# Performance work log

Measured on AMD Instinct MI355X. Metric: run time of the kernel, lower is better.

The kernel has to match this reference:

```python
import jax, jax.numpy as jnp
import numpy as np

HIDDEN = 2048
NUM_HEADS = 16
NUM_KV_HEADS = 4
HEAD_DIM = HIDDEN // NUM_HEADS  # 128
ROPE_THETA = 1000000.0
B, S = 2, 2048


def setup_inputs() -> dict:
    key = jax.random.key(0)
    ks = jax.random.split(key, 10)
    sc = 0.02
    return {
        "hidden_states": jax.random.normal(ks[0], (B, S, HIDDEN), jnp.float32),
        "position_ids": jnp.broadcast_to(jnp.arange(S, dtype=jnp.int32), (B, S)),
        "Wq": jax.random.normal(ks[1], (HIDDEN, NUM_HEADS * HEAD_DIM), jnp.float32) * sc,
        "bq": jnp.zeros((NUM_HEADS * HEAD_DIM,), jnp.float32),
        "Wk": jax.random.normal(ks[2], (HIDDEN, NUM_KV_HEADS * HEAD_DIM), jnp.float32) * sc,
        "bk": jnp.zeros((NUM_KV_HEADS * HEAD_DIM,), jnp.float32),
        "Wv": jax.random.normal(ks[3], (HIDDEN, NUM_KV_HEADS * HEAD_DIM), jnp.float32) * sc,
        "bv": jnp.zeros((NUM_KV_HEADS * HEAD_DIM,), jnp.float32),
        "Wo": jax.random.normal(ks[4], (NUM_HEADS * HEAD_DIM, HIDDEN), jnp.float32) * sc,
        "bo": jnp.zeros((HIDDEN,), jnp.float32),
    }


def _rope_cos_sin(position_ids, dtype):
    # inv_freq: [head_dim/2]
    inv_freq = 1.0 / (ROPE_THETA ** (jnp.arange(0, HEAD_DIM, 2, dtype=jnp.float32) / HEAD_DIM))
    freqs = position_ids.astype(jnp.float32)[:, :, None] * inv_freq[None, None, :]  # [B,S,d/2]
    emb = jnp.concatenate([freqs, freqs], axis=-1)  # [B,S,d]
    return jnp.cos(emb).astype(dtype), jnp.sin(emb).astype(dtype)


def _rotate_half(x):
    h = x.shape[-1] // 2
    return jnp.concatenate([-x[..., h:], x[..., :h]], axis=-1)


def _attention(hidden_states, position_ids, Wq, bq, Wk, bk, Wv, bv, Wo, bo):
    bsz, q_len, _ = hidden_states.shape
    q = (hidden_states @ Wq + bq).reshape(bsz, q_len, NUM_HEADS, HEAD_DIM).transpose(0, 2, 1, 3)
    k = (hidden_states @ Wk + bk).reshape(bsz, q_len, NUM_KV_HEADS, HEAD_DIM).transpose(0, 2, 1, 3)
    v = (hidden_states @ Wv + bv).reshape(bsz, q_len, NUM_KV_HEADS, HEAD_DIM).transpose(0, 2, 1, 3)

    cos, sin = _rope_cos_sin(position_ids, hidden_states.dtype)
    cos = cos[:, None, :, :]  # [B,1,S,d]
    sin = sin[:, None, :, :]
    q = q * cos + _rotate_half(q) * sin
    k = k * cos + _rotate_half(k) * sin

    # repeat_kv (GQA): [B,kvh,S,d] -> [B,H,S,d]
    n_rep = NUM_HEADS // NUM_KV_HEADS
    k = jnp.repeat(k, n_rep, axis=1)
    v = jnp.repeat(v, n_rep, axis=1)

    scale = 1.0 / jnp.sqrt(jnp.array(HEAD_DIM, hidden_states.dtype))
    scores = jnp.einsum('bhqd,bhkd->bhqk', q, k) * scale  # [B,H,S,S]
    causal = jnp.tril(jnp.ones((q_len, q_len), bool))
    scores = jnp.where(causal[None, None], scores, jnp.finfo(scores.dtype).min)
    probs = jax.nn.softmax(scores.astype(jnp.float32), axis=-1).astype(hidden_states.dtype)
    attn = jnp.einsum('bhqk,bhkd->bhqd', probs, v)
    attn = attn.transpose(0, 2, 1, 3).reshape(bsz, q_len, HIDDEN)
    return attn @ Wo + bo


def reference(hidden_states, position_ids, Wq, bq, Wk, bk, Wv, bv, Wo, bo):
    return _attention(hidden_states, position_ids, Wq, bq, Wk, bk, Wv, bv, Wo, bo)
```

## Files before the change

### kernel.cpp

```cpp
#include <hip/hip_runtime.h>
#include <cmath>

#define HIDDEN 2048
#define NH 16
#define NKV 4
#define HD 128
#define SEQ 2048
#define BATCH 2

typedef unsigned short ushort_t;
typedef short bf16x8 __attribute__((ext_vector_type(8)));
typedef float f32x4 __attribute__((ext_vector_type(4)));
typedef ushort_t u16x4 __attribute__((ext_vector_type(4)));

__device__ __forceinline__ ushort_t f2bf(float f) {
    union { float f; unsigned int u; } v; v.f = f;
    unsigned int r = v.u + 0x7fffu + ((v.u >> 16) & 1u);
    return (ushort_t)(r >> 16);
}
__device__ __forceinline__ ushort_t f2bf_trunc(float f) {
    union { float f; unsigned int u; } v; v.f = f;
    return (ushort_t)(v.u >> 16);
}

__device__ __forceinline__ f32x4 mfma16(bf16x8 a, bf16x8 b, f32x4 c) {
    return __builtin_amdgcn_mfma_f32_16x16x32_bf16(a, b, c, 0, 0, 0);
}

__device__ __forceinline__ void load_lds16(const void* g, void* l) {
    __builtin_amdgcn_global_load_lds((const __attribute__((address_space(1))) unsigned int*)g,
                                     (__attribute__((address_space(3))) unsigned int*)l,
                                     16, 0, 0);
}


__global__ __launch_bounds__(256) void prep(const float* __restrict__ Wq,
                                            const float* __restrict__ Wk,
                                            const float* __restrict__ Wv,
                                            const float* __restrict__ Wo,
                                            ushort_t* __restrict__ WqkvT,
                                            ushort_t* __restrict__ WoT,
                                            const float* __restrict__ hs,
                                            ushort_t* __restrict__ Xb) {
    const int z = blockIdx.z;
    const int t = threadIdx.x;
    if (z >= 4) {
        int g = (((z - 4) * 32 + blockIdx.y) * 32 + blockIdx.x) * 256 + t;
        float4 v = ((const float4*)hs)[g];
        u16x4 o;
        o[0] = f2bf(v.x); o[1] = f2bf(v.y); o[2] = f2bf(v.z); o[3] = f2bf(v.w);
        ((u16x4*)Xb)[g] = o;
        return;
    }
    const float* W;
    ushort_t* WT;
    int N;
    if (z == 0)      { W = Wq; WT = WqkvT;                        N = 2048; }
    else if (z == 1) { W = Wk; WT = WqkvT + 2048ull * 2048;       N = 512;  }
    else if (z == 2) { W = Wv; WT = WqkvT + 2560ull * 2048;       N = 512;  }
    else             { W = Wo; WT = WoT;                          N = 2048; }
    const int K = 2048;
    const int n0 = blockIdx.x * 64, k0 = blockIdx.y * 64;
    if (n0 >= N) return;
    __shared__ ushort_t T[64][72];
    for (int idx = t; idx < 64 * 16; idx += 256) {
        int r = idx >> 4, c4 = (idx & 15) << 2;
        float4 v = *(const float4*)&W[(size_t)(k0 + r) * N + n0 + c4];
        T[r][c4 + 0] = f2bf(v.x); T[r][c4 + 1] = f2bf(v.y);
        T[r][c4 + 2] = f2bf(v.z); T[r][c4 + 3] = f2bf(v.w);
    }
    __syncthreads();
    for (int idx = t; idx < 64 * 16; idx += 256) {
        int n = idx >> 4, kg = (idx & 15) << 2;
        u16x4 o;
        o[0] = T[kg + 0][n]; o[1] = T[kg + 1][n];
        o[2] = T[kg + 2][n]; o[3] = T[kg + 3][n];
        *(u16x4*)&WT[(size_t)(n0 + n) * K + k0 + kg] = o;
    }
}

template <int MODE, int BMH>
__global__ __launch_bounds__(512) void gemm256(const ushort_t* __restrict__ A,
                                               const ushort_t* __restrict__ Bt,
                                               const float* __restrict__ bias,
                                               const float* __restrict__ bias2,
                                               const float* __restrict__ bias3,
                                               void* __restrict__ out,
                                               void* __restrict__ out2,
                                               void* __restrict__ out3,
                                               int M, int N, int K,
                                               const int* __restrict__ posids) {
    constexpr int IM = 4 * BMH;
    constexpr int APL = BMH * 128 * 32;
    constexpr int BPL = 256 * 32;
    __shared__ __align__(16) ushort_t Asb[2 * 2 * APL];
    __shared__ __align__(16) ushort_t Bsb[2 * 2 * BPL];
    const int tid = threadIdx.x;
    const int w = tid >> 6, lane = tid & 63, quad = lane >> 4, l16 = lane & 15;
    const int wr = w >> 2, wc = w & 3;
    const int m0 = blockIdx.y * (128 * BMH), n0 = blockIdx.x * 256;

    f32x4 acc[IM][4];
#pragma unroll
    for (int i = 0; i < IM; i++)
#pragma unroll
        for (int j = 0; j < 4; j++)
#pragma unroll
            for (int e = 0; e < 4; e++) acc[i][j][e] = 0.0f;

    const int srow = lane >> 2;
    const int gc8 = (((lane & 3) ^ ((lane >> 3) & 3)) << 3);

    auto stageA = [&](int t, int buf, int ha) {
        const ushort_t* g = A + (size_t)(m0 + ha * 128 + w * 16 + srow) * K + t * 64 + gc8;
        ushort_t* l = &Asb[buf * 2 * APL + (ha * 128 + w * 16) * 32];
        load_lds16(g, l);
        load_lds16(g + 32, l + APL);
    };
    auto stageB = [&](int t, int buf, int ha) {
        const ushort_t* g = Bt + (size_t)(n0 + ha * 128 + w * 16 + srow) * K + t * 64 + gc8;
        ushort_t* l = &Bsb[buf * 2 * BPL + (ha * 128 + w * 16) * 32];
        load_lds16(g, l);
        load_lds16(g + 32, l + BPL);
    };

    const int slot = ((quad ^ ((l16 >> 1) & 3)) << 3);
    const int arow = (wr * (64 * BMH) + l16) * 32 + slot;
    const int brow = (wc * 16 + l16) * 32 + slot;

    const int nt = K >> 6;

    stageA(0, 0, 0);
    if constexpr (BMH == 2) stageA(0, 0, 1);
    stageB(0, 0, 0);
    stageB(0, 0, 1);
    asm volatile("s_waitcnt vmcnt(2)" ::: "memory");
    __builtin_amdgcn_s_barrier();
    __builtin_amdgcn_sched_barrier(0);

    bf16x8 a[IM];
    for (int u = 0; u < nt; ++u) {
        const int bu = u & 1, bn = bu ^ 1;
        const bool pf = (u + 1 < nt);
        const ushort_t* Ap0 = &Asb[bu * 2 * APL];
        const ushort_t* Ap1 = Ap0 + APL;
        const ushort_t* Bp0 = &Bsb[bu * 2 * BPL];
        const ushort_t* Bp1 = Bp0 + BPL;

#pragma unroll
        for (int i = 0; i < IM; i++) a[i] = *(const bf16x8*)&Ap0[arow + i * 512];
        bf16x8 b0 = *(const bf16x8*)&Bp0[brow];
        bf16x8 b1 = *(const bf16x8*)&Bp0[brow + 2048];
        if (pf) { stageA(u + 1, bn, 0); asm volatile("s_waitcnt vmcnt(2)" ::: "memory"); }
        else    { asm volatile("s_waitcnt vmcnt(0)" ::: "memory"); }
        __builtin_amdgcn_s_barrier();
        __builtin_amdgcn_sched_barrier(0);
        __builtin_amdgcn_s_setprio(1);
#pragma unroll
        for (int i = 0; i < IM; i++) {
            acc[i][0] = mfma16(a[i], b0, acc[i][0]);
            acc[i][1] = mfma16(a[i], b1, acc[i][1]);
        }
        __builtin_amdgcn_s_setprio(0);
        __builtin_amdgcn_sched_barrier(0);
        __builtin_amdgcn_s_barrier();
        __builtin_amdgcn_sched_barrier(0);

        bf16x8 b2 = *(const bf16x8*)&Bp0[brow + 4096];
        bf16x8 b3 = *(const bf16x8*)&Bp0[brow + 6144];
        if (pf) {
            if constexpr (BMH == 2) stageA(u + 1, bn, 1);
            else                    stageB(u + 1, bn, 0);
        }
        __builtin_amdgcn_s_barrier();
        __builtin_amdgcn_sched_barrier(0);
        __builtin_amdgcn_s_setprio(1);
#pragma unroll
        for (int i = 0; i < IM; i++) {
            acc[i][2] = mfma16(a[i], b2, acc[i][2]);
            acc[i][3] = mfma16(a[i], b3, acc[i][3]);
        }
        __builtin_amdgcn_s_setprio(0);
        __builtin_amdgcn_sched_barrier(0);
        __builtin_amdgcn_s_barrier();
        __builtin_amdgcn_sched_barrier(0);

#pragma unroll
        for (int i = 0; i < IM; i++) a[i] = *(const bf16x8*)&Ap1[arow + i * 512];
        b0 = *(const bf16x8*)&Bp1[brow];
        b1 = *(const bf16x8*)&Bp1[brow + 2048];
        if (pf) {
            if constexpr (BMH == 2) stageB(u + 1, bn, 0);
            else                    stageB(u + 1, bn, 1);
        }
        __builtin_amdgcn_s_barrier();
        __builtin_amdgcn_sched_barrier(0);
        __builtin_amdgcn_s_setprio(1);
#pragma unroll
        for (int i = 0; i < IM; i++) {
            acc[i][0] = mfma16(a[i], b0, acc[i][0]);
            acc[i][1] = mfma16(a[i], b1, acc[i][1]);
        }
        __builtin_amdgcn_s_setprio(0);
        __builtin_amdgcn_sched_barrier(0);
        __builtin_amdgcn_s_barrier();
        __builtin_amdgcn_sched_barrier(0);

        b2 = *(const bf16x8*)&Bp1[brow + 4096];
        b3 = *(const bf16x8*)&Bp1[brow + 6144];
        if (pf) {
            if constexpr (BMH == 2) stageB(u + 1, bn, 1);
            asm volatile("s_waitcnt vmcnt(2)" ::: "memory");
        }
        __builtin_amdgcn_s_barrier();
        __builtin_amdgcn_sched_barrier(0);
        __builtin_amdgcn_s_setprio(1);
#pragma unroll
        for (int i = 0; i < IM; i++) {
            acc[i][2] = mfma16(a[i], b2, acc[i][2]);
            acc[i][3] = mfma16(a[i], b3, acc[i][3]);
        }
        __builtin_amdgcn_s_setprio(0);
        __builtin_amdgcn_sched_barrier(0);
        __builtin_amdgcn_s_barrier();
        __builtin_amdgcn_sched_barrier(0);
    }

    if (MODE == 0) {
        float* O = (float*)out;
#pragma unroll
        for (int i = 0; i < IM; i++)
#pragma unroll
            for (int r = 0; r < 4; r++) {
                int row = m0 + wr * (64 * BMH) + i * 16 + quad * 4 + r;
#pragma unroll
                for (int j = 0; j < 4; j++) {
                    int col = n0 + (wc + 4 * j) * 16 + l16;
                    O[(size_t)row * N + col] = acc[i][j][r] + bias[col];
                }
            }
    } else {
        if (n0 < 2048) {
            ushort_t* O = (ushort_t*)out;
            const int h0 = n0 >> 7;
            const float scale = 0.08838834764831845f;
            const int dl = wc * 16 + l16;
            const float fr = __expf(-0.21586735246819178f * (float)dl);
#pragma unroll
            for (int i = 0; i < IM; i++)
#pragma unroll
                for (int r = 0; r < 4; r++) {
                    int row = m0 + wr * (64 * BMH) + i * 16 + quad * 4 + r;
                    int b = row >> 11, s = row & (SEQ - 1);
                    float pos = (float)posids[row];
                    float sn, cs;
                    __sincosf(pos * fr, &sn, &cs);
#pragma unroll
                    for (int p = 0; p < 2; p++) {
                        float x1 = acc[i][2 * p][r] + bias[n0 + p * 128 + dl];
                        float x2 = acc[i][2 * p + 1][r] + bias[n0 + p * 128 + dl + 64];
                        size_t obase = ((size_t)(b * NH + h0 + p) * SEQ + s) * HD;
                        O[obase + dl]      = f2bf((x1 * cs - x2 * sn) * scale);
                        O[obase + dl + 64] = f2bf((x2 * cs + x1 * sn) * scale);
                    }
                }
        } else if (n0 < 2560) {
            ushort_t* O = (ushort_t*)out2;
            const int n0k = n0 - 2048;
            const int h0 = n0k >> 7;
            const int dl = wc * 16 + l16;
            const float fr = __expf(-0.21586735246819178f * (float)dl);
#pragma unroll
            for (int i = 0; i < IM; i++)
#pragma unroll
                for (int r = 0; r < 4; r++) {
                    int row = m0 + wr * (64 * BMH) + i * 16 + quad * 4 + r;
                    int b = row >> 11, s = row & (SEQ - 1);
                    float pos = (float)posids[row];
                    float sn, cs;
                    __sincosf(pos * fr, &sn, &cs);
#pragma unroll
                    for (int p = 0; p < 2; p++) {
                        float x1 = acc[i][2 * p][r] + bias2[n0k + p * 128 + dl];
                        float x2 = acc[i][2 * p + 1][r] + bias2[n0k + p * 128 + dl + 64];
                        size_t obase = ((size_t)(b * NKV + h0 + p) * SEQ + s) * HD;
                        O[obase + dl]      = f2bf(x1 * cs - x2 * sn);
                        O[obase + dl + 64] = f2bf(x2 * cs + x1 * sn);
                    }
                }
        } else {
            ushort_t* O = (ushort_t*)out3;
            const int n0v = n0 - 2560;
#pragma unroll
            for (int i = 0; i < IM; i++)
#pragma unroll
                for (int r = 0; r < 4; r++) {
                    int row = m0 + wr * (64 * BMH) + i * 16 + quad * 4 + r;
                    int b = row >> 11, s = row & (SEQ - 1);
#pragma unroll
                    for (int j = 0; j < 4; j++) {
                        int ct = wc + 4 * j;
                        int h = (n0v >> 7) + (ct >> 3);
                        int d = (ct & 7) * 16 + l16;
                        float v = acc[i][j][r] + bias3[n0v + ct * 16 + l16];
                        O[((size_t)(b * NKV + h) * HD + d) * SEQ + s] = f2bf(v);
                    }
                }
        }
    }
}

__global__ __launch_bounds__(256) void flash(const ushort_t* __restrict__ Qr,
                                             const ushort_t* __restrict__ Kr,
                                             const ushort_t* __restrict__ Vt,
                                             ushort_t* __restrict__ Attn) {
    __shared__ __align__(16) ushort_t Ksh[2 * 4 * 64 * 32];
    __shared__ __align__(16) ushort_t Vsh[2 * 2 * 128 * 32];
    __shared__ __align__(16) ushort_t Ps[4 * 16 * 72];
    const int tid = threadIdx.x;
    const int w = tid >> 6, lane = tid & 63, quad = lane >> 4, l16 = lane & 15;
    const int x = blockIdx.x, h = blockIdx.y, b = blockIdx.z;
    const int qa = x, qb = 31 - x;
    const int nkt = qb + 1;
    const int hkv = h >> 2;
    const ushort_t* Kg = Kr + ((size_t)(b * NKV + hkv) * SEQ) * HD;
    const ushort_t* Vg = Vt + ((size_t)(b * NKV + hkv) * HD) * SEQ;

    const int p = lane >> 2;
    const int gc8 = (((lane & 3) ^ ((lane >> 3) & 3)) << 3);
    const ushort_t* kst = Kg + (size_t)p * HD + w * 32 + gc8;
    const ushort_t* vst = Vg + (size_t)((w & 1) * 64 + p) * SEQ + (w >> 1) * 32 + gc8;
    ushort_t* ksl = Ksh + w * 2048;
    ushort_t* vsl = Vsh + (w >> 1) * 4096 + (w & 1) * 2048;

    auto stage = [&](int bi, int kv0) {
        const ushort_t* gk = kst + (size_t)kv0 * HD;
        ushort_t* lk = ksl + bi * 8192;
        load_lds16(gk, lk);
        load_lds16(gk + (size_t)16 * HD, lk + 512);
        load_lds16(gk + (size_t)32 * HD, lk + 1024);
        load_lds16(gk + (size_t)48 * HD, lk + 1536);
        const ushort_t* gv = vst + kv0;
        ushort_t* lv = vsl + bi * 8192;
        load_lds16(gv, lv);
        load_lds16(gv + (size_t)16 * SEQ, lv + 512);
        load_lds16(gv + (size_t)32 * SEQ, lv + 1024);
        load_lds16(gv + (size_t)48 * SEQ, lv + 1536);
    };

    bf16x8 aq[2][4];
#pragma unroll
    for (int st = 0; st < 2; st++) {
        const int qst = st ? qb : qa;
        const size_t qrow = ((size_t)(b * NH + h) * SEQ + qst * 64 + w * 16 + l16) * HD;
#pragma unroll
        for (int kc = 0; kc < 4; kc++)
            aq[st][kc] = *(const bf16x8*)&Qr[qrow + kc * 32 + quad * 8];
    }

    f32x4 o[2][8];
#pragma unroll
    for (int st = 0; st < 2; st++)
#pragma unroll
        for (int j = 0; j < 8; j++)
#pragma unroll
            for (int e = 0; e < 4; e++) o[st][j][e] = 0.0f;
    f32x4 ls2[2];
#pragma unroll
    for (int st = 0; st < 2; st++)
        for (int e = 0; e < 4; e++) ls2[st][e] = 0.0f;
    bf16x8 ones;
#pragma unroll
    for (int e = 0; e < 8; e++) ones[e] = (short)0x3F80;

    ushort_t* Pw = &Ps[w * 16 * 72];
    const int rsw8 = ((l16 >> 1) & 3) << 3;

    stage(0, 0);
    asm volatile("s_waitcnt vmcnt(0)" ::: "memory");
    __builtin_amdgcn_s_barrier();

    for (int kt = 0; kt < nkt; kt++) {
        const int kv0 = kt * 64;
        const int cur = kt & 1;
        if (kt + 1 < nkt) {
            stage(cur ^ 1, kv0 + 64);
            asm volatile("s_waitcnt vmcnt(8)" ::: "memory");
        } else {
            asm volatile("s_waitcnt vmcnt(0)" ::: "memory");
        }
        __builtin_amdgcn_s_barrier();

        const ushort_t* Kb = Ksh + cur * 8192;
        const ushort_t* Vb = Vsh + cur * 8192;

#pragma unroll
        for (int st = 0; st < 2; st++) {
            const int qst = st ? qb : qa;
            if (st == 0 && kt > qa) continue;

            f32x4 sa[4];
#pragma unroll
            for (int nt = 0; nt < 4; nt++)
#pragma unroll
                for (int e = 0; e < 4; e++) sa[nt][e] = 0.0f;
#pragma unroll
            for (int kc = 0; kc < 4; kc++) {
#pragma unroll
                for (int nt = 0; nt < 4; nt++) {
                    bf16x8 bk = *(const bf16x8*)&Kb[kc * 2048 + nt * 512 + l16 * 32 +
                                                    ((quad * 8) ^ rsw8)];
                    sa[nt] = mfma16(aq[st][kc], bk, sa[nt]);
                }
            }

            if (kt == qst) {
#pragma unroll
                for (int nt = 0; nt < 4; nt++)
#pragma unroll
                    for (int r = 0; r < 4; r++) {
                        int kvg = kv0 + nt * 16 + l16;
                        int qg = qst * 64 + w * 16 + quad * 4 + r;
                        if (kvg > qg) sa[nt][r] = -1e30f;
                    }
            }

#pragma unroll
            for (int nt = 0; nt < 4; nt++)
#pragma unroll
                for (int r = 0; r < 4; r++)
                    Pw[(quad * 4 + r) * 72 + nt * 16 + l16] = f2bf_trunc(__expf(sa[nt][r]));

#pragma unroll
            for (int kc = 0; kc < 2; kc++) {
                bf16x8 ap = *(const bf16x8*)&Pw[l16 * 72 + kc * 32 + quad * 8];
                ls2[st] = mfma16(ap, ones, ls2[st]);
#pragma unroll
                for (int j = 0; j < 8; j++) {
                    bf16x8 bv = *(const bf16x8*)&Vb[kc * 4096 + (j * 16 + l16) * 32 +
                                                    ((quad * 8) ^ rsw8)];
                    o[st][j] = mfma16(ap, bv, o[st][j]);
                }
            }
        }
        asm volatile("s_barrier" ::: "memory");
    }

#pragma unroll
    for (int st = 0; st < 2; st++) {
        const int qst = st ? qb : qa;
#pragma unroll
        for (int r = 0; r < 4; r++) {
            float inv = 1.0f / ls2[st][r];
            int row = b * SEQ + qst * 64 + w * 16 + quad * 4 + r;
            size_t obase = (size_t)row * HIDDEN + h * HD;
#pragma unroll
            for (int j = 0; j < 8; j++) Attn[obase + j * 16 + l16] = f2bf(o[st][j][r] * inv);
        }
    }
}

extern "C" void kernel_launch(void* const* d_in, const int* in_sizes, int n_in,
                              void* d_out, int out_size, void* d_ws, size_t ws_size,
                              hipStream_t stream) {
    const float* hs = (const float*)d_in[0];
    const int* posids = (const int*)d_in[1];
    const float* Wq = (const float*)d_in[2];
    const float* bq = (const float*)d_in[3];
    const float* Wk = (const float*)d_in[4];
    const float* bk = (const float*)d_in[5];
    const float* Wv = (const float*)d_in[6];
    const float* bv = (const float*)d_in[7];
    const float* Wo = (const float*)d_in[8];
    const float* bo = (const float*)d_in[9];
    float* out = (float*)d_out;

    char* ws = (char*)d_ws;
    size_t off = 0;
    auto alloc = [&](size_t bytes) {
        char* p = ws + off;
        off += (bytes + 255) & ~(size_t)255;
        return p;
    };
    ushort_t* Xb     = (ushort_t*)alloc(4096ull * 2048 * 2);
    ushort_t* WqkvT  = (ushort_t*)alloc(3072ull * 2048 * 2);
    ushort_t* WoT    = (ushort_t*)alloc(2048ull * 2048 * 2);
    ushort_t* Qr     = (ushort_t*)alloc((size_t)BATCH * NH * SEQ * HD * 2);
    ushort_t* Kr     = (ushort_t*)alloc((size_t)BATCH * NKV * SEQ * HD * 2);
    ushort_t* Vtr    = (ushort_t*)alloc((size_t)BATCH * NKV * HD * SEQ * 2);
    ushort_t* Attn   = (ushort_t*)alloc(4096ull * 2048 * 2);

    prep<<<dim3(32, 32, 12), 256, 0, stream>>>(Wq, Wk, Wv, Wo, WqkvT, WoT, hs, Xb);

    gemm256<2, 2><<<dim3(12, 16), 512, 0, stream>>>(Xb, WqkvT, bq, bk, bv,
                                                    Qr, Kr, Vtr, 4096, 3072, 2048, posids);

    flash<<<dim3(16, NH, BATCH), 256, 0, stream>>>(Qr, Kr, Vtr, Attn);

    gemm256<0, 1><<<dim3(8, 32), 512, 0, stream>>>(Attn, WoT, bo, nullptr, nullptr,
                                                   out, nullptr, nullptr, 4096, 2048, 2048, nullptr);
}
```

Before: 298.7 us.

## Add dedicated QKV GEMM with 256x192 tiles and permuted weight columns for RoPE

Replaces the generic 256x256-tile QKV projection GEMM (12x16 = 192 blocks) with a specialized 256x192-tile kernel launched as 16x16 = 256 blocks, which fills the GPU's compute units more evenly. The prep kernel permutes Q/K weight columns so each wave's accumulators hold both RoPE halves (d and d+64) for a direct rotation in the epilogue. The new kernel uses a four-phase double-buffered LDS pipeline with interleaved prefetches. It adds a custom, harder-to-verify staging layout and more complex epilogue indexing.

After: 311.5 us. +4.3%, slower.

```diff
diff --git a/kernel.cpp b/kernel.cpp
--- a/kernel.cpp
+++ b/kernel.cpp
@@ -32,6 +32,7 @@
                                      (__attribute__((address_space(3))) unsigned int*)l,
                                      16, 0, 0);
 }
+
 
 
 __global__ __launch_bounds__(256) void prep(const float* __restrict__ Wq,
@@ -72,11 +73,218 @@
     __syncthreads();
     for (int idx = t; idx < 64 * 16; idx += 256) {
         int n = idx >> 4, kg = (idx & 15) << 2;
+        int c = n0 + n;
+        int pr = c;
+        if (z <= 1)
+            pr = (c & ~127) | ((((c >> 4) & 3) * 2 + ((c >> 6) & 1)) << 4) | (c & 15);
         u16x4 o;
         o[0] = T[kg + 0][n]; o[1] = T[kg + 1][n];
         o[2] = T[kg + 2][n]; o[3] = T[kg + 3][n];
-        *(u16x4*)&WT[(size_t)(n0 + n) * K + k0 + kg] = o;
-    }
+        *(u16x4*)&WT[(size_t)pr * K + k0 + kg] = o;
+    }
+}
+
+__global__ __launch_bounds__(512) void gemm_qkv(const ushort_t* __restrict__ A,
+                                                const ushort_t* __restrict__ Bt,
+                                                const float* __restrict__ bq,
+                                                const float* __restrict__ bk,
+                                                const float* __restrict__ bv,
+                                                ushort_t* __restrict__ Qr,
+                                                ushort_t* __restrict__ Kr,
+                                                ushort_t* __restrict__ Vt,
+                                                int K,
+                                                const int* __restrict__ posids) {
+    constexpr int APL = 256 * 32;
+    constexpr int BPL = 192 * 32;
+    __shared__ __align__(16) ushort_t Asb[2 * 2 * APL];
+    __shared__ __align__(16) ushort_t Bsb[2 * 2 * BPL];
+    const int tid = threadIdx.x;
+    const int w = tid >> 6, lane = tid & 63, quad = lane >> 4, l16 = lane & 15;
+    const int wr = w >> 1, wn = w & 1;
+    const int m0 = blockIdx.y * 256, n0 = blockIdx.x * 192;
+
+    f32x4 acc[4][6];
+#pragma unroll
+    for (int i = 0; i < 4; i++)
+#pragma unroll
+        for (int j = 0; j < 6; j++)
+#pragma unroll
+            for (int e = 0; e < 4; e++) acc[i][j][e] = 0.0f;
+
+    const int srow = lane >> 2;
+    const int gc8 = (((lane & 3) ^ ((lane >> 3) & 3)) << 3);
+
+    auto stageA = [&](int t, int buf, int ha) {
+        const ushort_t* g = A + (size_t)(m0 + ha * 128 + w * 16 + srow) * K + t * 64 + gc8;
+        ushort_t* l = &Asb[buf * 2 * APL + (ha * 128 + w * 16) * 32];
+        load_lds16(g, l);
+        load_lds16(g + 32, l + APL);
+    };
+    auto stageBa = [&](int t, int buf) {
+        const ushort_t* g = Bt + (size_t)(n0 + w * 16 + srow) * K + t * 64 + gc8;
+        load_lds16(g, &Bsb[buf * 2 * BPL + (w * 16) * 32]);
+    };
+    auto stageBb = [&](int t, int buf) {
+        const int r  = (w < 4) ? (128 + w * 16 + srow) : ((w - 4) * 16 + srow);
+        const int kc = (w < 4) ? 0 : 32;
+        const ushort_t* g = Bt + (size_t)(n0 + r) * K + t * 64 + kc + gc8;
+        load_lds16(g, &Bsb[buf * 2 * BPL + 4096 + w * 512]);
+    };
+    auto stageBc = [&](int t, int buf) {
+        const ushort_t* g = Bt + (size_t)(n0 + 64 + w * 16 + srow) * K + t * 64 + 32 + gc8;
+        load_lds16(g, &Bsb[buf * 2 * BPL + BPL + (64 + w * 16) * 32]);
+    };
+
+    const int slot = ((quad ^ ((l16 >> 1) & 3)) << 3);
+    const int arow = (wr * 64 + l16) * 32 + slot;
+    const int brow = (wn * 96 + l16) * 32 + slot;
+
+    const int nt = K >> 6;
+
+    stageA(0, 0, 0); stageA(0, 0, 1);
+    stageBa(0, 0); stageBb(0, 0); stageBc(0, 0);
+    asm volatile("s_waitcnt vmcnt(1)" ::: "memory");
+    __builtin_amdgcn_s_barrier();
+    __builtin_amdgcn_sched_barrier(0);
+
+    bf16x8 a[4];
+    for (int u = 0; u < nt; ++u) {
+        const int bu = u & 1, bn = bu ^ 1;
+        const bool pf = (u + 1 < nt);
+        const ushort_t* Ap0 = &Asb[bu * 2 * APL];
+        const ushort_t* Ap1 = Ap0 + APL;
+        const ushort_t* Bp0 = &Bsb[bu * 2 * BPL];
+        const ushort_t* Bp1 = Bp0 + BPL;
+
+#pragma unroll
+        for (int i = 0; i < 4; i++) a[i] = *(const bf16x8*)&Ap0[arow + i * 512];
+        bf16x8 b0 = *(const bf16x8*)&Bp0[brow];
+        bf16x8 b1 = *(const bf16x8*)&Bp0[brow + 512];
+        bf16x8 b2 = *(const bf16x8*)&Bp0[brow + 1024];
+        if (pf) { stageA(u + 1, bn, 0); asm volatile("s_waitcnt vmcnt(3)" ::: "memory"); }
+        else    { asm volatile("s_waitcnt vmcnt(0)" ::: "memory"); }
+        __builtin_amdgcn_s_barrier();
+        __builtin_amdgcn_sched_barrier(0);
+        __builtin_amdgcn_s_setprio(1);
+#pragma unroll
+        for (int i = 0; i < 4; i++) {
+            acc[i][0] = mfma16(a[i], b0, acc[i][0]);
+            acc[i][1] = mfma16(a[i], b1, acc[i][1]);
+            acc[i][2] = mfma16(a[i], b2, acc[i][2]);
+        }
+        __builtin_amdgcn_s_setprio(0);
+        __builtin_amdgcn_sched_barrier(0);
+        __builtin_amdgcn_s_barrier();
+        __builtin_amdgcn_sched_barrier(0);
+
+        bf16x8 b3 = *(const bf16x8*)&Bp0[brow + 1536];
+        bf16x8 b4 = *(const bf16x8*)&Bp0[brow + 2048];
+        bf16x8 b5 = *(const bf16x8*)&Bp0[brow + 2560];
+        if (pf) { stageA(u + 1, bn, 1); asm volatile("s_waitcnt vmcnt(4)" ::: "memory"); }
+        __builtin_amdgcn_s_barrier();
+        __builtin_amdgcn_sched_barrier(0);
+        __builtin_amdgcn_s_setprio(1);
+#pragma unroll
+        for (int i = 0; i < 4; i++) {
+            acc[i][3] = mfma16(a[i], b3, acc[i][3]);
+            acc[i][4] = mfma16(a[i], b4, acc[i][4]);
+            acc[i][5] = mfma16(a[i], b5, acc[i][5]);
+        }
+        __builtin_amdgcn_s_setprio(0);
+        __builtin_amdgcn_sched_barrier(0);
+        __builtin_amdgcn_s_barrier();
+        __builtin_amdgcn_sched_barrier(0);
+
+#pragma unroll
+        for (int i = 0; i < 4; i++) a[i] = *(const bf16x8*)&Ap1[arow + i * 512];
+        b0 = *(const bf16x8*)&Bp1[brow];
+        b1 = *(const bf16x8*)&Bp1[brow + 512];
+        b2 = *(const bf16x8*)&Bp1[brow + 1024];
+        if (pf) { stageBa(u + 1, bn); stageBb(u + 1, bn); }
+        __builtin_amdgcn_s_barrier();
+        __builtin_amdgcn_sched_barrier(0);
+        __builtin_amdgcn_s_setprio(1);
+#pragma unroll
+        for (int i = 0; i < 4; i++) {
+            acc[i][0] = mfma16(a[i], b0, acc[i][0]);
+            acc[i][1] = mfma16(a[i], b1, acc[i][1]);
+            acc[i][2] = mfma16(a[i], b2, acc[i][2]);
+        }
+        __builtin_amdgcn_s_setprio(0);
+        __builtin_amdgcn_sched_barrier(0);
+        __builtin_amdgcn_s_barrier();
+        __builtin_amdgcn_sched_barrier(0);
+
+        b3 = *(const bf16x8*)&Bp1[brow + 1536];
+        b4 = *(const bf16x8*)&Bp1[brow + 2048];
+        b5 = *(const bf16x8*)&Bp1[brow + 2560];
+        if (pf) stageBc(u + 1, bn);
+        __builtin_amdgcn_s_barrier();
+        __builtin_amdgcn_sched_barrier(0);
+        __builtin_amdgcn_s_setprio(1);
+#pragma unroll
+        for (int i = 0; i < 4; i++) {
+            acc[i][3] = mfma16(a[i], b3, acc[i][3]);
+            acc[i][4] = mfma16(a[i], b4, acc[i][4]);
+            acc[i][5] = mfma16(a[i], b5, acc[i][5]);
+        }
+        __builtin_amdgcn_s_setprio(0);
+        __builtin_amdgcn_sched_barrier(0);
+        __builtin_amdgcn_s_barrier();
+        __builtin_amdgcn_sched_barrier(0);
+    }
+
+    const float scale = 0.08838834764831845f;
+    int   dm_[3]; float fr_[3];
+#pragma unroll
+    for (int m = 0; m < 3; m++) {
+        int pcb = n0 + wn * 96 + m * 32;
+        dm_[m] = (((pcb < 2560 ? pcb : 0) >> 5) & 3) * 16 + l16;
+        fr_[m] = __expf(-0.21586735246819178f * (float)dm_[m]);
+    }
+#pragma unroll
+    for (int i = 0; i < 4; i++)
+#pragma unroll
+        for (int r = 0; r < 4; r++) {
+            int row = m0 + wr * 64 + i * 16 + quad * 4 + r;
+            int b = row >> 11, s = row & (SEQ - 1);
+            float pos = (float)posids[row];
+#pragma unroll
+            for (int m = 0; m < 3; m++) {
+                int pcb = n0 + wn * 96 + m * 32;
+                if (pcb < 2048) {
+                    int h = pcb >> 7;
+                    int d = dm_[m];
+                    float sn, cs;
+                    __sincosf(pos * fr_[m], &sn, &cs);
+                    float x1 = acc[i][2 * m][r]     + bq[h * 128 + d];
+                    float x2 = acc[i][2 * m + 1][r] + bq[h * 128 + d + 64];
+                    size_t ob = ((size_t)(b * NH + h) * SEQ + s) * HD;
+                    Qr[ob + d]      = f2bf((x1 * cs - x2 * sn) * scale);
+                    Qr[ob + d + 64] = f2bf((x2 * cs + x1 * sn) * scale);
+                } else if (pcb < 2560) {
+                    int c = pcb - 2048;
+                    int h = c >> 7;
+                    int d = dm_[m];
+                    float sn, cs;
+                    __sincosf(pos * fr_[m], &sn, &cs);
+                    float x1 = acc[i][2 * m][r]     + bk[h * 128 + d];
+                    float x2 = acc[i][2 * m + 1][r] + bk[h * 128 + d + 64];
+                    size_t ob = ((size_t)(b * NKV + h) * SEQ + s) * HD;
+                    Kr[ob + d]      = f2bf(x1 * cs - x2 * sn);
+                    Kr[ob + d + 64] = f2bf(x2 * cs + x1 * sn);
+                } else {
+#pragma unroll
+                    for (int q = 0; q < 2; q++) {
+                        int c = pcb + q * 16 - 2560;
+                        int h = c >> 7;
+                        int d = (c & 127) + l16;
+                        float v = acc[i][2 * m + q][r] + bv[c + l16];
+                        Vt[((size_t)(b * NKV + h) * HD + d) * SEQ + s] = f2bf(v);
+                    }
+                }
+            }
+        }
 }
 
 template <int MODE, int BMH>
@@ -239,74 +447,6 @@
                     O[(size_t)row * N + col] = acc[i][j][r] + bias[col];
                 }
             }
-    } else {
-        if (n0 < 2048) {
-            ushort_t* O = (ushort_t*)out;
-            const int h0 = n0 >> 7;
-            const float scale = 0.08838834764831845f;
-            const int dl = wc * 16 + l16;
-            const float fr = __expf(-0.21586735246819178f * (float)dl);
-#pragma unroll
-            for (int i = 0; i < IM; i++)
-#pragma unroll
-                for (int r = 0; r < 4; r++) {
-                    int row = m0 + wr * (64 * BMH) + i * 16 + quad * 4 + r;
-                    int b = row >> 11, s = row & (SEQ - 1);
-                    float pos = (float)posids[row];
-                    float sn, cs;
-                    __sincosf(pos * fr, &sn, &cs);
-#pragma unroll
-                    for (int p = 0; p < 2; p++) {
-                        float x1 = acc[i][2 * p][r] + bias[n0 + p * 128 + dl];
-                        float x2 = acc[i][2 * p + 1][r] + bias[n0 + p * 128 + dl + 64];
-                        size_t obase = ((size_t)(b * NH + h0 + p) * SEQ + s) * HD;
-                        O[obase + dl]      = f2bf((x1 * cs - x2 * sn) * scale);
-                        O[obase + dl + 64] = f2bf((x2 * cs + x1 * sn) * scale);
-                    }
-                }
-        } else if (n0 < 2560) {
-            ushort_t* O = (ushort_t*)out2;
-            const int n0k = n0 - 2048;
-            const int h0 = n0k >> 7;
-            const int dl = wc * 16 + l16;
-            const float fr = __expf(-0.21586735246819178f * (float)dl);
-#pragma unroll
-            for (int i = 0; i < IM; i++)
-#pragma unroll
-                for (int r = 0; r < 4; r++) {
-                    int row = m0 + wr * (64 * BMH) + i * 16 + quad * 4 + r;
-                    int b = row >> 11, s = row & (SEQ - 1);
-                    float pos = (float)posids[row];
-                    float sn, cs;
-                    __sincosf(pos * fr, &sn, &cs);
-#pragma unroll
-                    for (int p = 0; p < 2; p++) {
-                        float x1 = acc[i][2 * p][r] + bias2[n0k + p * 128 + dl];
-                        float x2 = acc[i][2 * p + 1][r] + bias2[n0k + p * 128 + dl + 64];
-                        size_t obase = ((size_t)(b * NKV + h0 + p) * SEQ + s) * HD;
-                        O[obase + dl]      = f2bf(x1 * cs - x2 * sn);
-                        O[obase + dl + 64] = f2bf(x2 * cs + x1 * sn);
-                    }
-                }
-        } else {
-            ushort_t* O = (ushort_t*)out3;
-            const int n0v = n0 - 2560;
-#pragma unroll
-            for (int i = 0; i < IM; i++)
-#pragma unroll
-                for (int r = 0; r < 4; r++) {
-                    int row = m0 + wr * (64 * BMH) + i * 16 + quad * 4 + r;
-                    int b = row >> 11, s = row & (SEQ - 1);
-#pragma unroll
-                    for (int j = 0; j < 4; j++) {
-                        int ct = wc + 4 * j;
-                        int h = (n0v >> 7) + (ct >> 3);
-                        int d = (ct & 7) * 16 + l16;
-                        float v = acc[i][j][r] + bias3[n0v + ct * 16 + l16];
-                        O[((size_t)(b * NKV + h) * HD + d) * SEQ + s] = f2bf(v);
-                    }
-                }
-        }
     }
 }
 
@@ -492,8 +632,8 @@
 
     prep<<<dim3(32, 32, 12), 256, 0, stream>>>(Wq, Wk, Wv, Wo, WqkvT, WoT, hs, Xb);
 
-    gemm256<2, 2><<<dim3(12, 16), 512, 0, stream>>>(Xb, WqkvT, bq, bk, bv,
-                                                    Qr, Kr, Vtr, 4096, 3072, 2048, posids);
+    gemm_qkv<<<dim3(16, 16), 512, 0, stream>>>(Xb, WqkvT, bq, bk, bv,
+                                               Qr, Kr, Vtr, 2048, posids);
 
     flash<<<dim3(16, NH, BATCH), 256, 0, stream>>>(Qr, Kr, Vtr, Attn);
 
```
